# Optimization experiments

Hardware: AMD Instinct MI355X
Metric: run time of the kernel (lower is better)

Reference implementation:

```python
import jax, jax.numpy as jnp
import numpy as np

D_MODEL = 256
N_HEADS = 8
HEAD_DIM = D_MODEL // N_HEADS  # 32
B, S = 8, 2048


def setup_inputs() -> dict:
    key = jax.random.key(0)
    ks = jax.random.split(key, 8)
    scale = 1.0 / np.sqrt(D_MODEL)
    return {
        "q": jax.random.normal(ks[0], (B, S, D_MODEL), jnp.float32),
        "k": jax.random.normal(ks[1], (B, S, D_MODEL), jnp.float32),
        "v": jax.random.normal(ks[2], (B, S, D_MODEL), jnp.float32),
        # padding mask: 1.0 = masked (added as -1e9), 0.0 = keep; shape (1,1,1,S)
        "m": jax.random.randint(ks[3], (1, 1, 1, S), 0, 2).astype(jnp.float32),
        "wq": jax.random.normal(ks[4], (D_MODEL, D_MODEL), jnp.float32) * scale,
        "bq": jnp.zeros((D_MODEL,), jnp.float32),
        "wk": jax.random.normal(ks[5], (D_MODEL, D_MODEL), jnp.float32) * scale,
        "bk": jnp.zeros((D_MODEL,), jnp.float32),
        "wv": jax.random.normal(ks[6], (D_MODEL, D_MODEL), jnp.float32) * scale,
        "bv": jnp.zeros((D_MODEL,), jnp.float32),
        "wo": jax.random.normal(ks[7], (D_MODEL, D_MODEL), jnp.float32) * scale,
        "bo": jnp.zeros((D_MODEL,), jnp.float32),
    }


def _split_heads(x):
    # (B, S, D) -> (B, H, S, dh)
    b, s, _ = x.shape
    return x.reshape(b, s, N_HEADS, HEAD_DIM).transpose(0, 2, 1, 3)


def reference(q, k, v, m, wq, bq, wk, bk, wv, bv, wo, bo):
    qh = _split_heads(q @ wq + bq)
    kh = _split_heads(k @ wk + bk)
    vh = _split_heads(v @ wv + bv)
    # scaled dot-product attention with additive padding mask
    logits = jnp.einsum("bhqd,bhkd->bhqk", qh, kh) / jnp.sqrt(
        jnp.asarray(HEAD_DIM, jnp.float32)
    )
    logits = logits + m * (-1e9)
    attn = jax.nn.softmax(logits, axis=-1)
    out = jnp.einsum("bhqk,bhkd->bhqd", attn, vh)  # (B, H, S, dh)
    out = out.transpose(0, 2, 1, 3).reshape(q.shape[0], -1, D_MODEL)
    return out @ wo + bo
```

## Files before the change

### kernel.cpp

```cpp
#include <hip/hip_runtime.h>

typedef short short8 __attribute__((ext_vector_type(8)));
typedef float f32x4 __attribute__((ext_vector_type(4)));
typedef float f32x16 __attribute__((ext_vector_type(16)));
typedef unsigned int uint2v __attribute__((ext_vector_type(2)));

#define NHEADS 8
#define DHEAD 32
#define DMODEL 256
#define SEQ 2048
#define QSCALE 0.17677669529663687f
#define LOG2E 1.4426950408889634f
#define NEGBIG -1.4427e9f
#define DEFER_THR 11.0f

__device__ __forceinline__ unsigned short f2bf(float x) {
  union { float f; unsigned int u; } c; c.f = x;
  return (unsigned short)((c.u + 0x7fffu + ((c.u >> 16) & 1u)) >> 16);
}

__device__ __forceinline__ unsigned int cvtpk(float lo, float hi) {
  unsigned int r;
  asm("v_cvt_pk_bf16_f32 %0, %1, %2" : "=v"(r) : "v"(lo), "v"(hi));
  return r;
}

__device__ __forceinline__ short8 pk8(float4 a, float4 b) {
  union { unsigned int u[4]; short8 s; } r;
  r.u[0] = cvtpk(a.x, a.y);
  r.u[1] = cvtpk(a.z, a.w);
  r.u[2] = cvtpk(b.x, b.y);
  r.u[3] = cvtpk(b.z, b.w);
  return r.s;
}

__device__ __forceinline__ float fexp2(float x) {
#if __has_builtin(__builtin_amdgcn_exp2f)
  return __builtin_amdgcn_exp2f(x);
#else
  return exp2f(x);
#endif
}

__device__ __forceinline__ uint2v plswap(unsigned int a, unsigned int b) {
#if __has_builtin(__builtin_amdgcn_permlane32_swap)
  return __builtin_amdgcn_permlane32_swap(a, b, false, false);
#else
  uint2v r;
  unsigned int sa = __shfl_xor(a, 32), sb = __shfl_xor(b, 32);
  int hi = (threadIdx.x & 63) >> 5;
  r[0] = hi ? sb : a;
  r[1] = hi ? b : sa;
  return r;
#endif
}

__device__ __forceinline__ int swz(int row, int c) {
  return row * 512 + ((c ^ (row & 7)) << 4);
}

__global__ __launch_bounds__(256) void prep_kernel(
    const float* __restrict__ wq, const float* __restrict__ wk,
    const float* __restrict__ wv, const float* __restrict__ wo,
    const float* __restrict__ bq, unsigned short* __restrict__ wt,
    float* __restrict__ bqs)
{
  __shared__ float tile[256][17];
  const int blk = blockIdx.x;
  const int mi = blk >> 4, nt = blk & 15;
  const float* w = (mi == 0) ? wq : (mi == 1) ? wk : (mi == 2) ? wv : wo;
  const float scale = (mi == 0) ? QSCALE * LOG2E : 1.0f;
  const int t = threadIdx.x;
  {
    const float* src = w + (size_t)t * DMODEL + nt * 16;
    #pragma unroll
    for (int i = 0; i < 16; i += 4) {
      float4 f = *(const float4*)(src + i);
      tile[t][i + 0] = f.x; tile[t][i + 1] = f.y;
      tile[t][i + 2] = f.z; tile[t][i + 3] = f.w;
    }
  }
  __syncthreads();
  unsigned short* dst = wt + mi * 65536 + nt * 4096;
  #pragma unroll
  for (int gi = 0; gi < 2; gi++) {
    const int g = t * 2 + gi;
    const int kk = g >> 6, l = g & 63;
    const int fr = l & 15, hi4 = l >> 4;
    union { unsigned short us[8]; uint4 u; } o;
    #pragma unroll
    for (int j = 0; j < 8; j++)
      o.us[j] = f2bf(tile[kk * 32 + hi4 * 8 + j][fr] * scale);
    *(uint4*)(dst + g * 8) = o.u;
  }
  if (blk == 0) bqs[t] = bq[t] * QSCALE * LOG2E;
}

__global__ __launch_bounds__(256) void scan_kernel(
    const float* __restrict__ m, int* __restrict__ cidx,
    float* __restrict__ tailbias, int* __restrict__ nkp)
{
  __shared__ int ssum[256];
  const int t = threadIdx.x;
  float mv[8];
  float4 m0 = *(const float4*)(m + t * 8);
  float4 m1 = *(const float4*)(m + t * 8 + 4);
  mv[0]=m0.x; mv[1]=m0.y; mv[2]=m0.z; mv[3]=m0.w;
  mv[4]=m1.x; mv[5]=m1.y; mv[6]=m1.z; mv[7]=m1.w;
  int keep[8], cnt = 0;
  #pragma unroll
  for (int j = 0; j < 8; j++) { keep[j] = (mv[j] == 0.0f); cnt += keep[j]; }
  ssum[t] = cnt;
  __syncthreads();
  for (int off = 1; off < 256; off <<= 1) {
    int add = (t >= off) ? ssum[t - off] : 0;
    __syncthreads();
    ssum[t] += add;
    __syncthreads();
  }
  int base = ssum[t] - cnt;
  const int nk = ssum[255];
  #pragma unroll
  for (int j = 0; j < 8; j++) {
    cidx[t * 8 + j] = keep[j] ? base : -1;
    base += keep[j];
  }
  if (t == 0) nkp[0] = nk;
  if (t < 32) {
    int g = (nk & ~31) + t;
    tailbias[t] = (g < nk) ? 0.0f : NEGBIG;
  }
}

__global__ __launch_bounds__(256) void qkv_kernel(
    const float* __restrict__ q, const float* __restrict__ k,
    const float* __restrict__ v, const unsigned short* __restrict__ wt,
    const float* __restrict__ bqs, const float* __restrict__ bk,
    const float* __restrict__ bv, const int* __restrict__ cidx,
    unsigned short* __restrict__ qf, unsigned short* __restrict__ kf,
    unsigned short* __restrict__ vf)
{
  __shared__ __align__(16) char alds[32768];
  const int z = blockIdx.y;
  const int tile = blockIdx.x;
  const int t = threadIdx.x;
  const int w = t >> 6, lane = t & 63;
  const int fr = lane & 15, hi4 = lane >> 4;

  const float* x = (z == 0) ? q : (z == 1) ? k : v;
  const float* xbase = x + (size_t)tile * 64 * DMODEL;

  #pragma unroll
  for (int i = 0; i < 8; i++) {
    const int gi = i * 256 + t;
    const int row = gi >> 5, c = gi & 31;
    const float4* src = (const float4*)(xbase + row * DMODEL + c * 8);
    float4 a0 = src[0], a1 = src[1];
    *(short8*)(alds + swz(row, c)) = pk8(a0, a1);
  }
  __syncthreads();

  f32x4 acc[4][4];
  #pragma unroll
  for (int mi = 0; mi < 4; mi++)
    #pragma unroll
    for (int ni = 0; ni < 4; ni++) { acc[mi][ni][0]=0.f; acc[mi][ni][1]=0.f; acc[mi][ni][2]=0.f; acc[mi][ni][3]=0.f; }

  const unsigned short* wz = wt + z * 65536 + (w * 4) * 4096;
  for (int kk = 0; kk < DMODEL; kk += 32) {
    short8 a[4], b[4];
    #pragma unroll
    for (int mi = 0; mi < 4; mi++)
      a[mi] = *(const short8*)(alds + swz(mi * 16 + fr, (kk >> 3) + hi4));
    #pragma unroll
    for (int ni = 0; ni < 4; ni++)
      b[ni] = *(const short8*)(wz + ni * 4096 + (kk >> 5) * 512 + lane * 8);
    if (z < 2) {
      #pragma unroll
      for (int mi = 0; mi < 4; mi++)
        #pragma unroll
        for (int ni = 0; ni < 4; ni++)
          acc[mi][ni] = __builtin_amdgcn_mfma_f32_16x16x32_bf16(b[ni], a[mi], acc[mi][ni], 0, 0, 0);
    } else {
      #pragma unroll
      for (int mi = 0; mi < 4; mi++)
        #pragma unroll
        for (int ni = 0; ni < 4; ni++)
          acc[mi][ni] = __builtin_amdgcn_mfma_f32_16x16x32_bf16(a[mi], b[ni], acc[mi][ni], 0, 0, 0);
    }
  }

  if (z < 2) {
    const float* bias = (z == 0) ? bqs : bk;
    unsigned short* dstbuf = (z == 0) ? qf : kf;
    float4 bias4[4];
    #pragma unroll
    for (int ni = 0; ni < 4; ni++)
      bias4[ni] = *(const float4*)(bias + w * 64 + ni * 16 + hi4 * 4);
    #pragma unroll
    for (int mi = 0; mi < 4; mi++) {
      const int tok = tile * 64 + mi * 16 + fr;
      const int b_ = tok >> 11, sl = tok & 2047;
      const int cs = (z == 0) ? sl : cidx[sl];
      if (cs >= 0) {
        #pragma unroll
        for (int ni = 0; ni < 4; ni++) {
          const int f0 = w * 64 + ni * 16 + hi4 * 4;
          const int h = f0 >> 5, dq = f0 & 31;
          uint2 val;
          val.x = cvtpk(acc[mi][ni][0] + bias4[ni].x, acc[mi][ni][1] + bias4[ni].y);
          val.y = cvtpk(acc[mi][ni][2] + bias4[ni].z, acc[mi][ni][3] + bias4[ni].w);
          const size_t off = (size_t)(b_ * NHEADS + h) * 65536
                           + (cs >> 5) * 1024 + ((dq >> 4) & 1) * 512 + ((dq >> 3) & 1) * 256
                           + (cs & 31) * 8 + (dq & 7);
          *(uint2*)(dstbuf + off) = val;
        }
      }
    }
  } else {
    #pragma unroll
    for (int ni = 0; ni < 4; ni++) {
      const int f = w * 64 + ni * 16 + fr;
      const float bb = bv[f];
      const int h = f >> 5, d = f & 31;
      #pragma unroll
      for (int mi = 0; mi < 4; mi++) {
        #pragma unroll
        for (int j = 0; j < 4; j++) {
          const int token = tile * 64 + mi * 16 + hi4 * 4 + j;
          const int b_ = token >> 11, s = token & 2047;
          const int cs = cidx[s];
          if (cs >= 0) {
            vf[(size_t)(b_ * NHEADS + h) * 65536
               + (cs >> 5) * 1024 + ((cs >> 4) & 1) * 512 + ((cs >> 3) & 1) * 256
               + d * 8 + (cs & 7)] = f2bf(acc[mi][ni][j] + bb);
          }
        }
      }
    }
  }
}

template<bool MASKED>
__device__ __forceinline__ void attn_tile(
    short8 kf0, short8 kf1, short8 vf0, short8 vf1, short8 onesf,
    short8 q0, short8 q1, const float* __restrict__ tailbias,
    int hi, f32x16& oacc, f32x16& lacc, float& mrun)
{
  f32x16 sacc;
  #pragma unroll
  for (int i = 0; i < 16; i++) sacc[i] = -mrun;
  __builtin_amdgcn_s_setprio(1);
  sacc = __builtin_amdgcn_mfma_f32_32x32x16_bf16(kf0, q0, sacc, 0, 0, 0);
  sacc = __builtin_amdgcn_mfma_f32_32x32x16_bf16(kf1, q1, sacc, 0, 0, 0);
  __builtin_amdgcn_s_setprio(0);

  float p[16];
  if (MASKED) {
    const float4 t0 = *(const float4*)(tailbias + 4 * hi);
    const float4 t1 = *(const float4*)(tailbias + 4 * hi + 8);
    const float4 t2 = *(const float4*)(tailbias + 4 * hi + 16);
    const float4 t3 = *(const float4*)(tailbias + 4 * hi + 24);
    p[0]=sacc[0]+t0.x;  p[1]=sacc[1]+t0.y;  p[2]=sacc[2]+t0.z;  p[3]=sacc[3]+t0.w;
    p[4]=sacc[4]+t1.x;  p[5]=sacc[5]+t1.y;  p[6]=sacc[6]+t1.z;  p[7]=sacc[7]+t1.w;
    p[8]=sacc[8]+t2.x;  p[9]=sacc[9]+t2.y;  p[10]=sacc[10]+t2.z; p[11]=sacc[11]+t2.w;
    p[12]=sacc[12]+t3.x; p[13]=sacc[13]+t3.y; p[14]=sacc[14]+t3.z; p[15]=sacc[15]+t3.w;
  } else {
    #pragma unroll
    for (int i = 0; i < 16; i++) p[i] = sacc[i];
  }

  float x0 = fmaxf(fmaxf(p[0], p[1]), p[2]);
  float x1 = fmaxf(fmaxf(p[3], p[4]), p[5]);
  float x2 = fmaxf(fmaxf(p[6], p[7]), p[8]);
  float x3 = fmaxf(fmaxf(p[9], p[10]), p[11]);
  float x4 = fmaxf(fmaxf(p[12], p[13]), p[14]);
  float tmax = fmaxf(fmaxf(fmaxf(x0, x1), fmaxf(x2, x3)), fmaxf(x4, p[15]));

  if (!__all(tmax <= DEFER_THR)) {
    float pm = fmaxf(tmax, __shfl_xor(tmax, 32));
    float delta = fmaxf(pm, 0.0f);
    float corr = fexp2(-delta);
    mrun += delta;
    lacc[0] *= corr;
    #pragma unroll
    for (int i = 0; i < 16; i++) oacc[i] *= corr;
    #pragma unroll
    for (int i = 0; i < 16; i++) p[i] -= delta;
  }

  #pragma unroll
  for (int i = 0; i < 16; i++) p[i] = fexp2(p[i]);

  const unsigned int A0 = cvtpk(p[0], p[1]);
  const unsigned int A1 = cvtpk(p[2], p[3]);
  const unsigned int B0 = cvtpk(p[4], p[5]);
  const unsigned int B1 = cvtpk(p[6], p[7]);
  const unsigned int A2 = cvtpk(p[8], p[9]);
  const unsigned int A3 = cvtpk(p[10], p[11]);
  const unsigned int B2 = cvtpk(p[12], p[13]);
  const unsigned int B3 = cvtpk(p[14], p[15]);
  union { unsigned int u[4]; short8 s; } pb0, pb1;
  uint2v r0 = plswap(A0, B0); pb0.u[0] = r0[0]; pb0.u[2] = r0[1];
  uint2v r1 = plswap(A1, B1); pb0.u[1] = r1[0]; pb0.u[3] = r1[1];
  uint2v r2 = plswap(A2, B2); pb1.u[0] = r2[0]; pb1.u[2] = r2[1];
  uint2v r3 = plswap(A3, B3); pb1.u[1] = r3[0]; pb1.u[3] = r3[1];

  __builtin_amdgcn_s_setprio(1);
  lacc = __builtin_amdgcn_mfma_f32_32x32x16_bf16(onesf, pb0.s, lacc, 0, 0, 0);
  lacc = __builtin_amdgcn_mfma_f32_32x32x16_bf16(onesf, pb1.s, lacc, 0, 0, 0);
  oacc = __builtin_amdgcn_mfma_f32_32x32x16_bf16(vf0, pb0.s, oacc, 0, 0, 0);
  oacc = __builtin_amdgcn_mfma_f32_32x32x16_bf16(vf1, pb1.s, oacc, 0, 0, 0);
  __builtin_amdgcn_s_setprio(0);
}

__global__ __launch_bounds__(256) void attn_kernel(
    const unsigned short* __restrict__ qf, const unsigned short* __restrict__ kfr,
    const unsigned short* __restrict__ vfr, const float* __restrict__ tailbias,
    const int* __restrict__ nkp, unsigned short* __restrict__ attno)
{
  const int bid = blockIdx.x;
  const int L = (bid & 7) * 128 + (bid >> 3);
  const int bh = L >> 4, qt = L & 15;
  const int w = threadIdx.x >> 6, lane = threadIdx.x & 63;
  const int ql = lane & 31, hi = lane >> 5;
  const int qrow = qt * 128 + w * 32 + ql;
  const int loff = hi * 256 + ql * 8;
  const unsigned short* Qb = qf + (size_t)bh * 65536 + (size_t)(qt * 4 + w) * 1024 + loff;
  const unsigned short* Kl = kfr + (size_t)bh * 65536 + loff;
  const unsigned short* Vl = vfr + (size_t)bh * 65536 + loff;

  const short8 q0 = *(const short8*)(Qb);
  const short8 q1 = *(const short8*)(Qb + 512);

  short8 onesf;
  #pragma unroll
  for (int i = 0; i < 8; i++) onesf[i] = (short)0x3F80;

  f32x16 oacc, lacc;
  #pragma unroll
  for (int i = 0; i < 16; i++) { oacc[i] = 0.0f; lacc[i] = 0.0f; }
  float mrun = 0.0f;

  const int nk = *nkp;
  const int nfull = nk >> 5, ntail = nk & 31;
  const int ntiles = nfull + (ntail ? 1 : 0);

  short8 ck0, ck1, cv0, cv1;
  if (ntiles > 0) {
    ck0 = *(const short8*)(Kl);
    ck1 = *(const short8*)(Kl + 512);
    cv0 = *(const short8*)(Vl);
    cv1 = *(const short8*)(Vl + 512);
  }
  for (int ti = 0; ti < nfull; ti++) {
    const int nb = (ti + 1 < ntiles ? ti + 1 : ti) * 1024;
    short8 nk0 = *(const short8*)(Kl + nb);
    short8 nk1 = *(const short8*)(Kl + nb + 512);
    short8 nv0 = *(const short8*)(Vl + nb);
    short8 nv1 = *(const short8*)(Vl + nb + 512);
    attn_tile<false>(ck0, ck1, cv0, cv1, onesf, q0, q1, tailbias, hi, oacc, lacc, mrun);
    ck0 = nk0; ck1 = nk1; cv0 = nv0; cv1 = nv1;
  }
  if (ntail)
    attn_tile<true>(ck0, ck1, cv0, cv1, onesf, q0, q1, tailbias, hi, oacc, lacc, mrun);

  const float inv = 1.0f / lacc[0];
  const int b = bh >> 3, h = bh & 7;
  unsigned short* orow = attno + ((size_t)(b * SEQ + qrow)) * DMODEL + h * DHEAD + 4 * hi;
  #pragma unroll
  for (int g = 0; g < 4; g++) {
    union { unsigned short us[4]; uint2 u2; } st;
    st.us[0] = f2bf(oacc[4 * g + 0] * inv);
    st.us[1] = f2bf(oacc[4 * g + 1] * inv);
    st.us[2] = f2bf(oacc[4 * g + 2] * inv);
    st.us[3] = f2bf(oacc[4 * g + 3] * inv);
    *(uint2*)(orow + 8 * g) = st.u2;
  }
}

__global__ __launch_bounds__(256) void oproj_kernel(
    const unsigned short* __restrict__ attno, const unsigned short* __restrict__ wto,
    const float* __restrict__ bo, float* __restrict__ out)
{
  __shared__ __align__(16) char alds[16384];
  const int tile = blockIdx.x;
  const int t = threadIdx.x;
  const int w = t >> 6, lane = t & 63;
  const int fr = lane & 15, hi4 = lane >> 4;
  const unsigned short* abase = attno + (size_t)tile * 32 * DMODEL;

  #pragma unroll
  for (int i = 0; i < 4; i++) {
    const int gi = i * 256 + t;
    const int row = gi >> 5, c = gi & 31;
    uint4 u = *(const uint4*)(abase + row * DMODEL + c * 8);
    *(uint4*)(alds + swz(row, c)) = u;
  }
  __syncthreads();

  f32x4 acc[2][4];
  #pragma unroll
  for (int mi = 0; mi < 2; mi++)
    #pragma unroll
    for (int ni = 0; ni < 4; ni++) { acc[mi][ni][0]=0.f; acc[mi][ni][1]=0.f; acc[mi][ni][2]=0.f; acc[mi][ni][3]=0.f; }

  const unsigned short* wz = wto + (w * 4) * 4096;
  for (int kk = 0; kk < DMODEL; kk += 32) {
    short8 a[2], b[4];
    #pragma unroll
    for (int mi = 0; mi < 2; mi++)
      a[mi] = *(const short8*)(alds + swz(mi * 16 + fr, (kk >> 3) + hi4));
    #pragma unroll
    for (int ni = 0; ni < 4; ni++)
      b[ni] = *(const short8*)(wz + ni * 4096 + (kk >> 5) * 512 + lane * 8);
    #pragma unroll
    for (int mi = 0; mi < 2; mi++)
      #pragma unroll
      for (int ni = 0; ni < 4; ni++)
        acc[mi][ni] = __builtin_amdgcn_mfma_f32_16x16x32_bf16(a[mi], b[ni], acc[mi][ni], 0, 0, 0);
  }

  #pragma unroll
  for (int ni = 0; ni < 4; ni++) {
    const int f = w * 64 + ni * 16 + fr;
    const float bb = bo[f];
    #pragma unroll
    for (int mi = 0; mi < 2; mi++) {
      #pragma unroll
      for (int j = 0; j < 4; j++) {
        const int token = tile * 32 + mi * 16 + hi4 * 4 + j;
        out[(size_t)token * DMODEL + f] = acc[mi][ni][j] + bb;
      }
    }
  }
}

extern "C" void kernel_launch(void* const* d_in, const int* in_sizes, int n_in,
                              void* d_out, int out_size, void* d_ws, size_t ws_size,
                              hipStream_t stream) {
  const float* q  = (const float*)d_in[0];
  const float* k  = (const float*)d_in[1];
  const float* v  = (const float*)d_in[2];
  const float* m  = (const float*)d_in[3];
  const float* wq = (const float*)d_in[4];
  const float* bq = (const float*)d_in[5];
  const float* wk = (const float*)d_in[6];
  const float* bk = (const float*)d_in[7];
  const float* wv = (const float*)d_in[8];
  const float* bv = (const float*)d_in[9];
  const float* wo = (const float*)d_in[10];
  const float* bo = (const float*)d_in[11];
  float* out = (float*)d_out;

  char* ws = (char*)d_ws;
  unsigned short* wt    = (unsigned short*)ws;
  float* bqs            = (float*)(ws + 524288);
  float* tailbias       = (float*)(ws + 525312);
  int*   nkp            = (int*)(ws + 525440);
  int*   cidx           = (int*)(ws + 526336);
  unsigned short* qf    = (unsigned short*)(ws + 1048576);
  unsigned short* kfr   = qf + 4194304;
  unsigned short* vfr   = kfr + 4194304;
  unsigned short* attno = vfr + 4194304;

  prep_kernel<<<dim3(64), dim3(256), 0, stream>>>(wq, wk, wv, wo, bq, wt, bqs);
  scan_kernel<<<dim3(1), dim3(256), 0, stream>>>(m, cidx, tailbias, nkp);
  qkv_kernel<<<dim3(256, 3), dim3(256), 0, stream>>>(q, k, v, wt, bqs, bk, bv, cidx, qf, kfr, vfr);
  attn_kernel<<<dim3(1024), dim3(256), 0, stream>>>(qf, kfr, vfr, tailbias, nkp, attno);
  oproj_kernel<<<dim3(512), dim3(256), 0, stream>>>(attno, wt + 3 * 65536, bo, out);
}
```

Baseline: 181.8 us.

## Fuse prep and scan kernels, shrink tiles, double-buffer attention K/V loads

Merges the weight-prep and mask-scan kernels into one launch to save a kernel launch. Halves the token tile in the QKV and output-projection GEMMs and halves the attention block to 128 threads with 64 query rows, doubling the grid in each case to spread work over more CUs. The attention loop now prefetches two K/V tiles ahead, alternating between two register sets, to hide global load latency. It also guards against a zero softmax denominator. Smaller tiles lower per-block reuse of the weight loads and add register pressure from the second K/V buffer.

```diff
diff --git a/kernel.cpp b/kernel.cpp
--- a/kernel.cpp
+++ b/kernel.cpp
@@ -59,76 +59,73 @@
   return row * 512 + ((c ^ (row & 7)) << 4);
 }
 
-__global__ __launch_bounds__(256) void prep_kernel(
+__global__ __launch_bounds__(256) void prep_scan_kernel(
     const float* __restrict__ wq, const float* __restrict__ wk,
     const float* __restrict__ wv, const float* __restrict__ wo,
-    const float* __restrict__ bq, unsigned short* __restrict__ wt,
-    float* __restrict__ bqs)
+    const float* __restrict__ bq, const float* __restrict__ m,
+    unsigned short* __restrict__ wt, float* __restrict__ bqs,
+    int* __restrict__ cidx, float* __restrict__ tailbias, int* __restrict__ nkp)
 {
   __shared__ float tile[256][17];
+  __shared__ int ssum[256];
   const int blk = blockIdx.x;
-  const int mi = blk >> 4, nt = blk & 15;
-  const float* w = (mi == 0) ? wq : (mi == 1) ? wk : (mi == 2) ? wv : wo;
-  const float scale = (mi == 0) ? QSCALE * LOG2E : 1.0f;
   const int t = threadIdx.x;
-  {
-    const float* src = w + (size_t)t * DMODEL + nt * 16;
-    #pragma unroll
-    for (int i = 0; i < 16; i += 4) {
-      float4 f = *(const float4*)(src + i);
-      tile[t][i + 0] = f.x; tile[t][i + 1] = f.y;
-      tile[t][i + 2] = f.z; tile[t][i + 3] = f.w;
-    }
-  }
-  __syncthreads();
-  unsigned short* dst = wt + mi * 65536 + nt * 4096;
-  #pragma unroll
-  for (int gi = 0; gi < 2; gi++) {
-    const int g = t * 2 + gi;
-    const int kk = g >> 6, l = g & 63;
-    const int fr = l & 15, hi4 = l >> 4;
-    union { unsigned short us[8]; uint4 u; } o;
-    #pragma unroll
-    for (int j = 0; j < 8; j++)
-      o.us[j] = f2bf(tile[kk * 32 + hi4 * 8 + j][fr] * scale);
-    *(uint4*)(dst + g * 8) = o.u;
-  }
-  if (blk == 0) bqs[t] = bq[t] * QSCALE * LOG2E;
-}
-
-__global__ __launch_bounds__(256) void scan_kernel(
-    const float* __restrict__ m, int* __restrict__ cidx,
-    float* __restrict__ tailbias, int* __restrict__ nkp)
-{
-  __shared__ int ssum[256];
-  const int t = threadIdx.x;
-  float mv[8];
-  float4 m0 = *(const float4*)(m + t * 8);
-  float4 m1 = *(const float4*)(m + t * 8 + 4);
-  mv[0]=m0.x; mv[1]=m0.y; mv[2]=m0.z; mv[3]=m0.w;
-  mv[4]=m1.x; mv[5]=m1.y; mv[6]=m1.z; mv[7]=m1.w;
-  int keep[8], cnt = 0;
-  #pragma unroll
-  for (int j = 0; j < 8; j++) { keep[j] = (mv[j] == 0.0f); cnt += keep[j]; }
-  ssum[t] = cnt;
-  __syncthreads();
-  for (int off = 1; off < 256; off <<= 1) {
-    int add = (t >= off) ? ssum[t - off] : 0;
+  if (blk < 64) {
+    const int mi = blk >> 4, nt = blk & 15;
+    const float* w = (mi == 0) ? wq : (mi == 1) ? wk : (mi == 2) ? wv : wo;
+    const float scale = (mi == 0) ? QSCALE * LOG2E : 1.0f;
+    {
+      const float* src = w + (size_t)t * DMODEL + nt * 16;
+      #pragma unroll
+      for (int i = 0; i < 16; i += 4) {
+        float4 f = *(const float4*)(src + i);
+        tile[t][i + 0] = f.x; tile[t][i + 1] = f.y;
+        tile[t][i + 2] = f.z; tile[t][i + 3] = f.w;
+      }
+    }
     __syncthreads();
-    ssum[t] += add;
+    unsigned short* dst = wt + mi * 65536 + nt * 4096;
+    #pragma unroll
+    for (int gi = 0; gi < 2; gi++) {
+      const int g = t * 2 + gi;
+      const int kk = g >> 6, l = g & 63;
+      const int fr = l & 15, hi4 = l >> 4;
+      union { unsigned short us[8]; uint4 u; } o;
+      #pragma unroll
+      for (int j = 0; j < 8; j++)
+        o.us[j] = f2bf(tile[kk * 32 + hi4 * 8 + j][fr] * scale);
+      *(uint4*)(dst + g * 8) = o.u;
+    }
+    if (blk == 0) bqs[t] = bq[t] * QSCALE * LOG2E;
+  } else {
+    float mv[8];
+    float4 m0 = *(const float4*)(m + t * 8);
+    float4 m1 = *(const float4*)(m + t * 8 + 4);
+    mv[0]=m0.x; mv[1]=m0.y; mv[2]=m0.z; mv[3]=m0.w;
+    mv[4]=m1.x; mv[5]=m1.y; mv[6]=m1.z; mv[7]=m1.w;
+    int keep[8], cnt = 0;
+    #pragma unroll
+    for (int j = 0; j < 8; j++) { keep[j] = (mv[j] == 0.0f); cnt += keep[j]; }
+    ssum[t] = cnt;
     __syncthreads();
-  }
-  int base = ssum[t] - cnt;
-  const int nk = ssum[255];
-  #pragma unroll
-  for (int j = 0; j < 8; j++) {
-    cidx[t * 8 + j] = keep[j] ? base : -1;
-    base += keep[j];
-  }
-  if (t == 0) nkp[0] = nk;
-  if (t < 32) {
-    int g = (nk & ~31) + t;
-    tailbias[t] = (g < nk) ? 0.0f : NEGBIG;
+    for (int off = 1; off < 256; off <<= 1) {
+      int add = (t >= off) ? ssum[t - off] : 0;
+      __syncthreads();
+      ssum[t] += add;
+      __syncthreads();
+    }
+    int base = ssum[t] - cnt;
+    const int nk = ssum[255];
+    #pragma unroll
+    for (int j = 0; j < 8; j++) {
+      cidx[t * 8 + j] = keep[j] ? base : -1;
+      base += keep[j];
+    }
+    if (t == 0) nkp[0] = nk;
+    if (t < 32) {
+      int g = (nk & ~31) + t;
+      tailbias[t] = (g < nk) ? 0.0f : NEGBIG;
+    }
   }
 }
 
@@ -140,7 +137,7 @@
     unsigned short* __restrict__ qf, unsigned short* __restrict__ kf,
     unsigned short* __restrict__ vf)
 {
-  __shared__ __align__(16) char alds[32768];
+  __shared__ __align__(16) char alds[16384];
   const int z = blockIdx.y;
   const int tile = blockIdx.x;
   const int t = threadIdx.x;
@@ -148,10 +145,10 @@
   const int fr = lane & 15, hi4 = lane >> 4;
 
   const float* x = (z == 0) ? q : (z == 1) ? k : v;
-  const float* xbase = x + (size_t)tile * 64 * DMODEL;
-
-  #pragma unroll
-  for (int i = 0; i < 8; i++) {
+  const float* xbase = x + (size_t)tile * 32 * DMODEL;
+
+  #pragma unroll
+  for (int i = 0; i < 4; i++) {
     const int gi = i * 256 + t;
     const int row = gi >> 5, c = gi & 31;
     const float4* src = (const float4*)(xbase + row * DMODEL + c * 8);
@@ -160,30 +157,30 @@
   }
   __syncthreads();
 
-  f32x4 acc[4][4];
-  #pragma unroll
-  for (int mi = 0; mi < 4; mi++)
+  f32x4 acc[2][4];
+  #pragma unroll
+  for (int mi = 0; mi < 2; mi++)
     #pragma unroll
     for (int ni = 0; ni < 4; ni++) { acc[mi][ni][0]=0.f; acc[mi][ni][1]=0.f; acc[mi][ni][2]=0.f; acc[mi][ni][3]=0.f; }
 
   const unsigned short* wz = wt + z * 65536 + (w * 4) * 4096;
   for (int kk = 0; kk < DMODEL; kk += 32) {
-    short8 a[4], b[4];
-    #pragma unroll
-    for (int mi = 0; mi < 4; mi++)
+    short8 a[2], b[4];
+    #pragma unroll
+    for (int mi = 0; mi < 2; mi++)
       a[mi] = *(const short8*)(alds + swz(mi * 16 + fr, (kk >> 3) + hi4));
     #pragma unroll
     for (int ni = 0; ni < 4; ni++)
       b[ni] = *(const short8*)(wz + ni * 4096 + (kk >> 5) * 512 + lane * 8);
     if (z < 2) {
       #pragma unroll
-      for (int mi = 0; mi < 4; mi++)
+      for (int mi = 0; mi < 2; mi++)
         #pragma unroll
         for (int ni = 0; ni < 4; ni++)
           acc[mi][ni] = __builtin_amdgcn_mfma_f32_16x16x32_bf16(b[ni], a[mi], acc[mi][ni], 0, 0, 0);
     } else {
       #pragma unroll
-      for (int mi = 0; mi < 4; mi++)
+      for (int mi = 0; mi < 2; mi++)
         #pragma unroll
         for (int ni = 0; ni < 4; ni++)
           acc[mi][ni] = __builtin_amdgcn_mfma_f32_16x16x32_bf16(a[mi], b[ni], acc[mi][ni], 0, 0, 0);
@@ -198,8 +195,8 @@
     for (int ni = 0; ni < 4; ni++)
       bias4[ni] = *(const float4*)(bias + w * 64 + ni * 16 + hi4 * 4);
     #pragma unroll
-    for (int mi = 0; mi < 4; mi++) {
-      const int tok = tile * 64 + mi * 16 + fr;
+    for (int mi = 0; mi < 2; mi++) {
+      const int tok = tile * 32 + mi * 16 + fr;
       const int b_ = tok >> 11, sl = tok & 2047;
       const int cs = (z == 0) ? sl : cidx[sl];
       if (cs >= 0) {
@@ -224,10 +221,10 @@
       const float bb = bv[f];
       const int h = f >> 5, d = f & 31;
       #pragma unroll
-      for (int mi = 0; mi < 4; mi++) {
+      for (int mi = 0; mi < 2; mi++) {
         #pragma unroll
         for (int j = 0; j < 4; j++) {
-          const int token = tile * 64 + mi * 16 + hi4 * 4 + j;
+          const int token = tile * 32 + mi * 16 + hi4 * 4 + j;
           const int b_ = token >> 11, s = token & 2047;
           const int cs = cidx[s];
           if (cs >= 0) {
@@ -314,19 +311,19 @@
   __builtin_amdgcn_s_setprio(0);
 }
 
-__global__ __launch_bounds__(256) void attn_kernel(
+__global__ __launch_bounds__(128) void attn_kernel(
     const unsigned short* __restrict__ qf, const unsigned short* __restrict__ kfr,
     const unsigned short* __restrict__ vfr, const float* __restrict__ tailbias,
     const int* __restrict__ nkp, unsigned short* __restrict__ attno)
 {
   const int bid = blockIdx.x;
-  const int L = (bid & 7) * 128 + (bid >> 3);
-  const int bh = L >> 4, qt = L & 15;
+  const int L = (bid & 7) * 256 + (bid >> 3);
+  const int bh = L >> 5, qt = L & 31;
   const int w = threadIdx.x >> 6, lane = threadIdx.x & 63;
   const int ql = lane & 31, hi = lane >> 5;
-  const int qrow = qt * 128 + w * 32 + ql;
+  const int qrow = qt * 64 + w * 32 + ql;
   const int loff = hi * 256 + ql * 8;
-  const unsigned short* Qb = qf + (size_t)bh * 65536 + (size_t)(qt * 4 + w) * 1024 + loff;
+  const unsigned short* Qb = qf + (size_t)bh * 65536 + (size_t)(qt * 2 + w) * 1024 + loff;
   const unsigned short* Kl = kfr + (size_t)bh * 65536 + loff;
   const unsigned short* Vl = vfr + (size_t)bh * 65536 + loff;
 
@@ -345,27 +342,50 @@
   const int nk = *nkp;
   const int nfull = nk >> 5, ntail = nk & 31;
   const int ntiles = nfull + (ntail ? 1 : 0);
-
-  short8 ck0, ck1, cv0, cv1;
-  if (ntiles > 0) {
-    ck0 = *(const short8*)(Kl);
-    ck1 = *(const short8*)(Kl + 512);
-    cv0 = *(const short8*)(Vl);
-    cv1 = *(const short8*)(Vl + 512);
-  }
-  for (int ti = 0; ti < nfull; ti++) {
-    const int nb = (ti + 1 < ntiles ? ti + 1 : ti) * 1024;
-    short8 nk0 = *(const short8*)(Kl + nb);
-    short8 nk1 = *(const short8*)(Kl + nb + 512);
-    short8 nv0 = *(const short8*)(Vl + nb);
-    short8 nv1 = *(const short8*)(Vl + nb + 512);
-    attn_tile<false>(ck0, ck1, cv0, cv1, onesf, q0, q1, tailbias, hi, oacc, lacc, mrun);
-    ck0 = nk0; ck1 = nk1; cv0 = nv0; cv1 = nv1;
-  }
-  if (ntail)
-    attn_tile<true>(ck0, ck1, cv0, cv1, onesf, q0, q1, tailbias, hi, oacc, lacc, mrun);
-
-  const float inv = 1.0f / lacc[0];
+  const int last = (ntiles > 0) ? (ntiles - 1) : 0;
+
+  short8 ak0 = *(const short8*)(Kl);
+  short8 ak1 = *(const short8*)(Kl + 512);
+  short8 av0 = *(const short8*)(Vl);
+  short8 av1 = *(const short8*)(Vl + 512);
+  const int nb1 = ((1 <= last) ? 1 : last) * 1024;
+  short8 bk0 = *(const short8*)(Kl + nb1);
+  short8 bk1 = *(const short8*)(Kl + nb1 + 512);
+  short8 bv0 = *(const short8*)(Vl + nb1);
+  short8 bv1 = *(const short8*)(Vl + nb1 + 512);
+
+  int ti = 0;
+  while (ti + 2 <= nfull) {
+    attn_tile<false>(ak0, ak1, av0, av1, onesf, q0, q1, tailbias, hi, oacc, lacc, mrun);
+    {
+      const int nt = (ti + 2 <= last) ? (ti + 2) : last;
+      const int nb = nt * 1024;
+      ak0 = *(const short8*)(Kl + nb);
+      ak1 = *(const short8*)(Kl + nb + 512);
+      av0 = *(const short8*)(Vl + nb);
+      av1 = *(const short8*)(Vl + nb + 512);
+    }
+    attn_tile<false>(bk0, bk1, bv0, bv1, onesf, q0, q1, tailbias, hi, oacc, lacc, mrun);
+    {
+      const int nt = (ti + 3 <= last) ? (ti + 3) : last;
+      const int nb = nt * 1024;
+      bk0 = *(const short8*)(Kl + nb);
+      bk1 = *(const short8*)(Kl + nb + 512);
+      bv0 = *(const short8*)(Vl + nb);
+      bv1 = *(const short8*)(Vl + nb + 512);
+    }
+    ti += 2;
+  }
+  if (ti < nfull) {
+    attn_tile<false>(ak0, ak1, av0, av1, onesf, q0, q1, tailbias, hi, oacc, lacc, mrun);
+    if (ntail)
+      attn_tile<true>(bk0, bk1, bv0, bv1, onesf, q0, q1, tailbias, hi, oacc, lacc, mrun);
+  } else if (ntail) {
+    attn_tile<true>(ak0, ak1, av0, av1, onesf, q0, q1, tailbias, hi, oacc, lacc, mrun);
+  }
+
+  const float den = lacc[0];
+  const float inv = (den > 0.0f) ? (1.0f / den) : 0.0f;
   const int b = bh >> 3, h = bh & 7;
   unsigned short* orow = attno + ((size_t)(b * SEQ + qrow)) * DMODEL + h * DHEAD + 4 * hi;
   #pragma unroll
@@ -383,15 +403,15 @@
     const unsigned short* __restrict__ attno, const unsigned short* __restrict__ wto,
     const float* __restrict__ bo, float* __restrict__ out)
 {
-  __shared__ __align__(16) char alds[16384];
+  __shared__ __align__(16) char alds[8192];
   const int tile = blockIdx.x;
   const int t = threadIdx.x;
   const int w = t >> 6, lane = t & 63;
   const int fr = lane & 15, hi4 = lane >> 4;
-  const unsigned short* abase = attno + (size_t)tile * 32 * DMODEL;
-
-  #pragma unroll
-  for (int i = 0; i < 4; i++) {
+  const unsigned short* abase = attno + (size_t)tile * 16 * DMODEL;
+
+  #pragma unroll
+  for (int i = 0; i < 2; i++) {
     const int gi = i * 256 + t;
     const int row = gi >> 5, c = gi & 31;
     uint4 u = *(const uint4*)(abase + row * DMODEL + c * 8);
@@ -399,26 +419,20 @@
   }
   __syncthreads();
 
-  f32x4 acc[2][4];
-  #pragma unroll
-  for (int mi = 0; mi < 2; mi++)
-    #pragma unroll
-    for (int ni = 0; ni < 4; ni++) { acc[mi][ni][0]=0.f; acc[mi][ni][1]=0.f; acc[mi][ni][2]=0.f; acc[mi][ni][3]=0.f; }
+  f32x4 acc[4];
+  #pragma unroll
+  for (int ni = 0; ni < 4; ni++) { acc[ni][0]=0.f; acc[ni][1]=0.f; acc[ni][2]=0.f; acc[ni][3]=0.f; }
 
   const unsigned short* wz = wto + (w * 4) * 4096;
   for (int kk = 0; kk < DMODEL; kk += 32) {
-    short8 a[2], b[4];
-    #pragma unroll
-    for (int mi = 0; mi < 2; mi++)
-      a[mi] = *(const short8*)(alds + swz(mi * 16 + fr, (kk >> 3) + hi4));
+    short8 a = *(const short8*)(alds + swz(fr, (kk >> 3) + hi4));
+    short8 b[4];
     #pragma unroll
     for (int ni = 0; ni < 4; ni++)
       b[ni] = *(const short8*)(wz + ni * 4096 + (kk >> 5) * 512 + lane * 8);
     #pragma unroll
-    for (int mi = 0; mi < 2; mi++)
-      #pragma unroll
-      for (int ni = 0; ni < 4; ni++)
-        acc[mi][ni] = __builtin_amdgcn_mfma_f32_16x16x32_bf16(a[mi], b[ni], acc[mi][ni], 0, 0, 0);
+    for (int ni = 0; ni < 4; ni++)
+      acc[ni] = __builtin_amdgcn_mfma_f32_16x16x32_bf16(a, b[ni], acc[ni], 0, 0, 0);
   }
 
   #pragma unroll
@@ -426,12 +440,9 @@
     const int f = w * 64 + ni * 16 + fr;
     const float bb = bo[f];
     #pragma unroll
-    for (int mi = 0; mi < 2; mi++) {
-      #pragma unroll
-      for (int j = 0; j < 4; j++) {
-        const int token = tile * 32 + mi * 16 + hi4 * 4 + j;
-        out[(size_t)token * DMODEL + f] = acc[mi][ni][j] + bb;
-      }
+    for (int j = 0; j < 4; j++) {
+      const int token = tile * 16 + hi4 * 4 + j;
+      out[(size_t)token * DMODEL + f] = acc[ni][j] + bb;
     }
   }
 }
@@ -464,9 +475,8 @@
   unsigned short* vfr   = kfr + 4194304;
   unsigned short* attno = vfr + 4194304;
 
-  prep_kernel<<<dim3(64), dim3(256), 0, stream>>>(wq, wk, wv, wo, bq, wt, bqs);
-  scan_kernel<<<dim3(1), dim3(256), 0, stream>>>(m, cidx, tailbias, nkp);
-  qkv_kernel<<<dim3(256, 3), dim3(256), 0, stream>>>(q, k, v, wt, bqs, bk, bv, cidx, qf, kfr, vfr);
-  attn_kernel<<<dim3(1024), dim3(256), 0, stream>>>(qf, kfr, vfr, tailbias, nkp, attno);
-  oproj_kernel<<<dim3(512), dim3(256), 0, stream>>>(attno, wt + 3 * 65536, bo, out);
-}
+  prep_scan_kernel<<<dim3(65), dim3(256), 0, stream>>>(wq, wk, wv, wo, bq, m, wt, bqs, cidx, tailbias, nkp);
+  qkv_kernel<<<dim3(512, 3), dim3(256), 0, stream>>>(q, k, v, wt, bqs, bk, bv, cidx, qf, kfr, vfr);
+  attn_kernel<<<dim3(2048), dim3(128), 0, stream>>>(qf, kfr, vfr, tailbias, nkp, attno);
+  oproj_kernel<<<dim3(1024), dim3(256), 0, stream>>>(attno, wt + 3 * 65536, bo, out);
+}
```

Measured after the change: 176.6 us. -2.9%, faster.
